# Optimization experiments

Measured on AMD Instinct MI355X. Metric: run time of the kernel, lower is better.

Reference implementation:

```python
import jax, jax.numpy as jnp
import numpy as np

EPS = 1e-10
TEMP = 1.0
N_ITERS = 21  # 20 + int(1.0 / temp)


def _sinkhorn(log_alpha, temp, n_iters):
    # log_alpha: (..., n, n). Alternating row/col log-normalization in log space.
    la = log_alpha / temp
    for _ in range(n_iters):
        la = la - jax.scipy.special.logsumexp(la, axis=-2, keepdims=True)
        la = la - jax.scipy.special.logsumexp(la, axis=-1, keepdims=True)
    return jnp.exp(la)


def setup_inputs() -> dict:
    key = jax.random.key(0)
    k1, k2, k3 = jax.random.split(key, 3)
    B, N, S = 256, 1024, 16
    x = jax.random.normal(k1, (B, N), dtype=jnp.float32)
    log_alpha = jax.random.normal(k2, (N, N), dtype=jnp.float32)  # learned param (init was gumbel noise)
    u = jax.random.uniform(k3, (S, N, N), dtype=jnp.float32)  # uniform draws for Gumbel noise
    return {"x": x, "log_alpha": log_alpha, "u": u}


def reference(x, log_alpha, u):
    # Gumbel noise from uniform draws: -log(eps - log(U + eps))
    noise = -jnp.log(EPS - jnp.log(u + EPS))  # (S, N, N)
    log_alpha_noise = log_alpha[None, :, :] + noise
    soft_perms = _sinkhorn(log_alpha_noise, TEMP, N_ITERS)  # (S, N, N)
    # x: (B, N) -> (1, B, N) @ (S, N, N) -> (S, B, N)
    return jnp.einsum('bn,snm->sbm', x, soft_perms)
```

## Files before the change

### kernel.cpp

```cpp
#include <hip/hip_runtime.h>
#include <math.h>

static constexpr int S_ = 16;
static constexpr int N_ = 1024;
static constexpr int B_ = 256;
static constexpr int ITERS = 21;
#define EPSC 1e-10f

using short8 = __attribute__((ext_vector_type(8))) short;
using f32x4  = __attribute__((ext_vector_type(4))) float;

__device__ __forceinline__ float bf2f(unsigned short h) {
    union { unsigned int u; float f; } v; v.u = ((unsigned int)h) << 16; return v.f;
}
__device__ __forceinline__ unsigned short f2bf(float f) {
    union { float f; unsigned int u; } v; v.f = f;
    unsigned int r = v.u + 0x7fffu + ((v.u >> 16) & 1u);
    return (unsigned short)(r >> 16);
}
__device__ __forceinline__ unsigned int pack2(float a, float b) {
    return (unsigned int)f2bf(a) | ((unsigned int)f2bf(b) << 16);
}

__device__ __forceinline__ float la0_of(float uv, float lav) {
    float t1 = __logf(uv + EPSC);
    float t2 = EPSC - t1;
    return lav - __logf(t2);
}

__device__ __forceinline__ void unpack16(const uint4& a, const uint4& b, float* kf) {
    kf[0]  = bf2f((unsigned short)(a.x & 0xffffu)); kf[1]  = bf2f((unsigned short)(a.x >> 16));
    kf[2]  = bf2f((unsigned short)(a.y & 0xffffu)); kf[3]  = bf2f((unsigned short)(a.y >> 16));
    kf[4]  = bf2f((unsigned short)(a.z & 0xffffu)); kf[5]  = bf2f((unsigned short)(a.z >> 16));
    kf[6]  = bf2f((unsigned short)(a.w & 0xffffu)); kf[7]  = bf2f((unsigned short)(a.w >> 16));
    kf[8]  = bf2f((unsigned short)(b.x & 0xffffu)); kf[9]  = bf2f((unsigned short)(b.x >> 16));
    kf[10] = bf2f((unsigned short)(b.y & 0xffffu)); kf[11] = bf2f((unsigned short)(b.y >> 16));
    kf[12] = bf2f((unsigned short)(b.z & 0xffffu)); kf[13] = bf2f((unsigned short)(b.z >> 16));
    kf[14] = bf2f((unsigned short)(b.w & 0xffffu)); kf[15] = bf2f((unsigned short)(b.w >> 16));
}

__global__ void __launch_bounds__(256)
build_K2(const float* __restrict__ u, const float* __restrict__ la,
         unsigned short* __restrict__ Kb, float* __restrict__ partial) {
    const int bid = blockIdx.x;
    const int s    = (bid & 7) + 8 * ((bid >> 3) & 1);
    const int slab = bid >> 4;
    const int t = threadIdx.x, wv = t >> 6, l = t & 63;
    const int i0 = slab * 8 + wv * 2;

    float cs[16];
    #pragma unroll
    for (int e = 0; e < 16; ++e) cs[e] = 0.f;

    f32x4 uu[2][4];
    float4 ll[2][4];
    #pragma unroll
    for (int rr = 0; rr < 2; ++rr) {
        const int i = i0 + rr;
        const float* up  = u  + ((size_t)s * N_ + i) * N_ + 8 * l;
        const float* lap = la + (size_t)i * N_ + 8 * l;
        uu[rr][0] = __builtin_nontemporal_load((const f32x4*)(up));
        uu[rr][1] = __builtin_nontemporal_load((const f32x4*)(up + 4));
        uu[rr][2] = __builtin_nontemporal_load((const f32x4*)(up + 512));
        uu[rr][3] = __builtin_nontemporal_load((const f32x4*)(up + 516));
        ll[rr][0] = *(const float4*)(lap);
        ll[rr][1] = *(const float4*)(lap + 4);
        ll[rr][2] = *(const float4*)(lap + 512);
        ll[rr][3] = *(const float4*)(lap + 516);
    }
    #pragma unroll
    for (int rr = 0; rr < 2; ++rr) {
        const int i = i0 + rr;
        #pragma unroll
        for (int h = 0; h < 2; ++h) {
            const float uf[8] = {uu[rr][2*h][0], uu[rr][2*h][1], uu[rr][2*h][2], uu[rr][2*h][3],
                                 uu[rr][2*h+1][0], uu[rr][2*h+1][1], uu[rr][2*h+1][2], uu[rr][2*h+1][3]};
            const float lf[8] = {ll[rr][2*h].x, ll[rr][2*h].y, ll[rr][2*h].z, ll[rr][2*h].w,
                                 ll[rr][2*h+1].x, ll[rr][2*h+1].y, ll[rr][2*h+1].z, ll[rr][2*h+1].w};
            unsigned int pk[4];
            #pragma unroll
            for (int e = 0; e < 4; ++e) {
                float k0 = __expf(lf[2*e])   / (EPSC - __logf(uf[2*e]   + EPSC));
                float k1 = __expf(lf[2*e+1]) / (EPSC - __logf(uf[2*e+1] + EPSC));
                unsigned short b0 = f2bf(k0), b1 = f2bf(k1);
                pk[e] = (unsigned int)b0 | ((unsigned int)b1 << 16);
                cs[h*8 + 2*e]     += bf2f(b0);
                cs[h*8 + 2*e + 1] += bf2f(b1);
            }
            *(uint4*)(Kb + ((size_t)s * N_ + i) * N_ + h * 512 + 8 * l) =
                make_uint4(pk[0], pk[1], pk[2], pk[3]);
        }
    }

    __shared__ float lds[4][1024];
    *(float4*)&lds[wv][8*l]           = make_float4(cs[0], cs[1], cs[2], cs[3]);
    *(float4*)&lds[wv][8*l + 4]       = make_float4(cs[4], cs[5], cs[6], cs[7]);
    *(float4*)&lds[wv][512 + 8*l]     = make_float4(cs[8], cs[9], cs[10], cs[11]);
    *(float4*)&lds[wv][512 + 8*l + 4] = make_float4(cs[12], cs[13], cs[14], cs[15]);
    __syncthreads();
    const int j = t * 4;
    float4 p0 = *(const float4*)&lds[0][j];
    float4 p1 = *(const float4*)&lds[1][j];
    float4 p2 = *(const float4*)&lds[2][j];
    float4 p3 = *(const float4*)&lds[3][j];
    float4 o;
    o.x = p0.x + p1.x + p2.x + p3.x;  o.y = p0.y + p1.y + p2.y + p3.y;
    o.z = p0.z + p1.z + p2.z + p3.z;  o.w = p0.w + p1.w + p2.w + p3.w;
    *(float4*)(partial + ((size_t)s * 128 + slab) * N_ + j) = o;
}

template<int NS>
__global__ void __launch_bounds__(256)
reduce_V(const float* __restrict__ partial, float* __restrict__ V) {
    const int s = blockIdx.x >> 2;
    const int j = (blockIdx.x & 3) * 256 + threadIdx.x;
    const float* p = partial + (size_t)s * NS * N_ + j;
    float acc = 0.f;
    #pragma unroll
    for (int q = 0; q < NS; ++q) acc += p[(size_t)q * N_];
    V[s * N_ + j] = 1.0f / acc;
}

__global__ void __launch_bounds__(256)
sink_iter(const unsigned short* __restrict__ Kb, const float* __restrict__ V,
          float* __restrict__ U, float* __restrict__ partial, int do_colsum) {
    const int bid = blockIdx.x;
    const int s    = (bid & 7) + 8 * ((bid >> 3) & 1);
    const int slab = bid >> 4;
    const int t = threadIdx.x, wv = t >> 6, l = t & 63;

    float v[16];
    const float* Vp = V + s * N_;
    *(float4*)&v[0]  = *(const float4*)(Vp + 8*l);
    *(float4*)&v[4]  = *(const float4*)(Vp + 8*l + 4);
    *(float4*)&v[8]  = *(const float4*)(Vp + 512 + 8*l);
    *(float4*)&v[12] = *(const float4*)(Vp + 512 + 8*l + 4);

    float cs[16];
    #pragma unroll
    for (int e = 0; e < 16; ++e) cs[e] = 0.f;

    const int i0 = slab * 16 + wv * 4;
    const unsigned short* rowp = Kb + ((size_t)s * N_ + i0) * N_;
    #pragma unroll
    for (int rr = 0; rr < 4; ++rr, rowp += N_) {
        uint4 ra = *(const uint4*)(rowp + 8*l);
        uint4 rb = *(const uint4*)(rowp + 512 + 8*l);
        float kf[16];
        unpack16(ra, rb, kf);
        float dot = 0.f;
        #pragma unroll
        for (int e = 0; e < 16; ++e) dot += kf[e] * v[e];
        #pragma unroll
        for (int m = 32; m >= 1; m >>= 1) dot += __shfl_xor(dot, m);
        const float ui = 1.0f / dot;
        if (l == 0) U[s * N_ + i0 + rr] = ui;
        #pragma unroll
        for (int e = 0; e < 16; ++e) cs[e] += kf[e] * ui;
    }

    if (!do_colsum) return;
    __shared__ float lds[4][1024];
    *(float4*)&lds[wv][8*l]           = make_float4(cs[0], cs[1], cs[2], cs[3]);
    *(float4*)&lds[wv][8*l + 4]       = make_float4(cs[4], cs[5], cs[6], cs[7]);
    *(float4*)&lds[wv][512 + 8*l]     = make_float4(cs[8], cs[9], cs[10], cs[11]);
    *(float4*)&lds[wv][512 + 8*l + 4] = make_float4(cs[12], cs[13], cs[14], cs[15]);
    __syncthreads();
    const int j = t * 4;
    float4 p0 = *(const float4*)&lds[0][j];
    float4 p1 = *(const float4*)&lds[1][j];
    float4 p2 = *(const float4*)&lds[2][j];
    float4 p3 = *(const float4*)&lds[3][j];
    float4 o;
    o.x = p0.x + p1.x + p2.x + p3.x;  o.y = p0.y + p1.y + p2.y + p3.y;
    o.z = p0.z + p1.z + p2.z + p3.z;  o.w = p0.w + p1.w + p2.w + p3.w;
    *(float4*)(partial + ((size_t)s * 64 + slab) * N_ + j) = o;
}

__global__ void __launch_bounds__(256)
transpose_K(const unsigned short* __restrict__ Kb, unsigned short* __restrict__ KbT) {
    const int s = blockIdx.z, k0 = blockIdx.x * 64, m0 = blockIdx.y * 64;
    __shared__ unsigned short tile[64][66];
    const int t = threadIdx.x, c4 = (t & 15) * 4, rr = t >> 4;
    const unsigned short* src = Kb + (size_t)s * N_ * N_;
    unsigned short* dst = KbT + (size_t)s * N_ * N_;
    #pragma unroll
    for (int q = 0; q < 4; ++q) {
        const int r = q * 16 + rr;
        ushort4 v = *(const ushort4*)(src + (size_t)(k0 + r) * N_ + m0 + c4);
        tile[r][c4] = v.x; tile[r][c4 + 1] = v.y; tile[r][c4 + 2] = v.z; tile[r][c4 + 3] = v.w;
    }
    __syncthreads();
    #pragma unroll
    for (int q = 0; q < 4; ++q) {
        const int rm = q * 16 + rr;
        ushort4 v;
        v.x = tile[c4][rm]; v.y = tile[c4 + 1][rm];
        v.z = tile[c4 + 2][rm]; v.w = tile[c4 + 3][rm];
        *(ushort4*)(dst + (size_t)(m0 + rm) * N_ + k0 + c4) = v;
    }
}

__global__ void __launch_bounds__(512)
mfma_out(const float* __restrict__ x, const unsigned short* __restrict__ KbT,
         const float* __restrict__ U, const float* __restrict__ V,
         float* __restrict__ out) {
    const int s  = blockIdx.z;
    const int m0 = blockIdx.x * 64;
    const int b0 = blockIdx.y * 128;
    const int t  = threadIdx.x;
    const int wid = t >> 6, l = t & 63;
    const int wr = wid & 3;
    const int wc = wid >> 2;

    __shared__ alignas(16) unsigned short lsA[128 * 64];
    __shared__ alignas(16) unsigned short lsB[64 * 64];

    f32x4 acc[2][2];
    #pragma unroll
    for (int fi = 0; fi < 2; ++fi)
        #pragma unroll
        for (int fj = 0; fj < 2; ++fj)
            acc[fi][fj] = (f32x4){0.f, 0.f, 0.f, 0.f};

    const unsigned short* Bp = KbT + ((size_t)s * N_ + m0) * N_;
    const float* Up = U + s * N_;

    float4 xa[2], xb[2];
    uint4  kv;
    float4 ua, ub;

    auto load_tile = [&](int k0) {
        #pragma unroll
        for (int i = 0; i < 2; ++i) {
            const int Lb  = i * 8192 + t * 16;
            const int row = Lb >> 7;
            const int kb  = Lb & 127;
            const float* xp = x + (size_t)(b0 + row) * N_ + k0 + (kb >> 1);
            xa[i] = *(const float4*)xp;
            xb[i] = *(const float4*)(xp + 4);
        }
        {
            const int Lb  = t * 16;
            const int row = Lb >> 7;
            const int kb  = Lb & 127;
            kv = *(const uint4*)((const char*)Bp + (size_t)row * 2048 + (k0 << 1) + kb);
            const int ke = k0 + (kb >> 1);
            ua = *(const float4*)(Up + ke);
            ub = *(const float4*)(Up + ke + 4);
        }
    };

    load_tile(0);
    for (int k0 = 0; k0 < N_; k0 += 64) {
        __syncthreads();
        #pragma unroll
        for (int i = 0; i < 2; ++i) {
            const int Lb  = i * 8192 + t * 16;
            const int row = Lb >> 7;
            const int kb  = Lb & 127;
            uint4 pk = make_uint4(pack2(xa[i].x, xa[i].y), pack2(xa[i].z, xa[i].w),
                                  pack2(xb[i].x, xb[i].y), pack2(xb[i].z, xb[i].w));
            *(uint4*)((char*)lsA + (row << 7) + (kb ^ ((row & 7) << 4))) = pk;
        }
        {
            const int Lb  = t * 16;
            const int row = Lb >> 7;
            const int kb  = Lb & 127;
            uint4 pk;
            pk.x = pack2(bf2f((unsigned short)(kv.x & 0xffffu)) * ua.x,
                         bf2f((unsigned short)(kv.x >> 16))     * ua.y);
            pk.y = pack2(bf2f((unsigned short)(kv.y & 0xffffu)) * ua.z,
                         bf2f((unsigned short)(kv.y >> 16))     * ua.w);
            pk.z = pack2(bf2f((unsigned short)(kv.z & 0xffffu)) * ub.x,
                         bf2f((unsigned short)(kv.z >> 16))     * ub.y);
            pk.w = pack2(bf2f((unsigned short)(kv.w & 0xffffu)) * ub.z,
                         bf2f((unsigned short)(kv.w >> 16))     * ub.w);
            *(uint4*)((char*)lsB + (row << 7) + (kb ^ ((row & 7) << 4))) = pk;
        }
        __syncthreads();
        if (k0 + 64 < N_) load_tile(k0 + 64);
        #pragma unroll
        for (int ks = 0; ks < 2; ++ks) {
            const int koff = ks * 64 + ((l >> 4) << 4);
            short8 afr[2], bfr[2];
            #pragma unroll
            for (int fi = 0; fi < 2; ++fi) {
                const int r = wr * 32 + fi * 16 + (l & 15);
                afr[fi] = *(const short8*)((const char*)lsA + (r << 7) + (koff ^ ((r & 7) << 4)));
            }
            #pragma unroll
            for (int fj = 0; fj < 2; ++fj) {
                const int r = wc * 32 + fj * 16 + (l & 15);
                bfr[fj] = *(const short8*)((const char*)lsB + (r << 7) + (koff ^ ((r & 7) << 4)));
            }
            #pragma unroll
            for (int fi = 0; fi < 2; ++fi)
                #pragma unroll
                for (int fj = 0; fj < 2; ++fj)
                    acc[fi][fj] = __builtin_amdgcn_mfma_f32_16x16x32_bf16(
                        afr[fi], bfr[fj], acc[fi][fj], 0, 0, 0);
        }
    }
    #pragma unroll
    for (int fj = 0; fj < 2; ++fj) {
        const int m = m0 + wc * 32 + fj * 16 + (l & 15);
        const float vm = V[s * N_ + m];
        #pragma unroll
        for (int fi = 0; fi < 2; ++fi) {
            const int b = b0 + wr * 32 + fi * 16 + ((l >> 4) << 2);
            float* op = out + ((size_t)s * B_ + b) * N_ + m;
            #pragma unroll
            for (int e = 0; e < 4; ++e)
                op[(size_t)e * N_] = acc[fi][fj][e] * vm;
        }
    }
}

__global__ void __launch_bounds__(256)
transpose_x(const float* __restrict__ x, float* __restrict__ xT) {
    __shared__ float tile[32][33];
    const int tx = threadIdx.x, ty = threadIdx.y;
    const int gx = blockIdx.x * 32, gy = blockIdx.y * 32;
    #pragma unroll
    for (int i = 0; i < 4; ++i)
        tile[ty + i * 8][tx] = x[(gy + ty + i * 8) * N_ + gx + tx];
    __syncthreads();
    #pragma unroll
    for (int i = 0; i < 4; ++i)
        xT[(size_t)(gx + ty + i * 8) * B_ + gy + tx] = tile[tx][ty + i * 8];
}

__global__ void __launch_bounds__(256)
col_pass(const float* __restrict__ u, const float* __restrict__ la,
         const float* __restrict__ r, float* __restrict__ c) {
    const int s = blockIdx.y, t = threadIdx.x;
    const int tx = t & 15, rg = t >> 4;
    const int j = blockIdx.x * 16 + tx;
    __shared__ alignas(16) float r_lds[N_];
    ((float4*)r_lds)[t] = ((const float4*)(r + s * N_))[t];
    __syncthreads();
    const float cj = c[s * N_ + j];
    const float* up = u + (size_t)s * N_ * N_;
    const int i0 = rg * 64;
    float acc = 0.f;
    #pragma unroll 4
    for (int ii = 0; ii < 64; ++ii) {
        const int i = i0 + ii;
        acc += __expf(la0_of(up[(size_t)i * N_ + j], la[i * N_ + j]) - r_lds[i] - cj);
    }
    __shared__ float sums[16][17];
    sums[rg][tx] = acc;
    __syncthreads();
    if (t < 16) {
        float tot = 0.f;
        #pragma unroll
        for (int k = 0; k < 16; ++k) tot += sums[k][t];
        c[s * N_ + blockIdx.x * 16 + t] = cj + __logf(tot);
    }
}

__global__ void __launch_bounds__(256)
row_pass(const float* __restrict__ u, const float* __restrict__ la,
         const float* __restrict__ c, float* __restrict__ r) {
    const int s = blockIdx.y, t = threadIdx.x;
    const int w = t >> 6, l = t & 63;
    const int i = blockIdx.x * 4 + w;
    __shared__ alignas(16) float c_lds[N_];
    ((float4*)c_lds)[t] = ((const float4*)(c + s * N_))[t];
    __syncthreads();
    const float ri = r[s * N_ + i];
    const float* up = u + (size_t)s * N_ * N_ + (size_t)i * N_;
    const float* lap = la + (size_t)i * N_;
    float acc = 0.f;
    #pragma unroll
    for (int k = 0; k < 16; ++k) {
        const int jj = l + (k << 6);
        acc += __expf(la0_of(up[jj], lap[jj]) - c_lds[jj] - ri);
    }
    #pragma unroll
    for (int m = 32; m >= 1; m >>= 1) acc += __shfl_xor(acc, m);
    if (l == 0) r[s * N_ + i] = ri + __logf(acc);
}

__global__ void __launch_bounds__(256)
matmul_out(const float* __restrict__ u, const float* __restrict__ la,
           const float* __restrict__ xT, const float* __restrict__ r,
           const float* __restrict__ c, float* __restrict__ out) {
    const int s = blockIdx.z, m0 = blockIdx.x * 64, b0 = blockIdx.y * 128;
    const int t = threadIdx.x, tx = t & 7, ty = t >> 3;
    __shared__ alignas(16) float Bs[16][64];
    float acc[4][8] = {};
    const float* up = u + (size_t)s * N_ * N_;
    const float* rp = r + s * N_;
    for (int k0 = 0; k0 < N_; k0 += 16) {
        __syncthreads();
        {
            const int kk = t >> 4, f4 = t & 15;
            const int k = k0 + kk;
            const float rk = rp[k];
            const float4 uv = *(const float4*)(up + (size_t)k * N_ + m0 + f4 * 4);
            const float4 lv = *(const float4*)(la + (size_t)k * N_ + m0 + f4 * 4);
            float4 p;
            p.x = __expf(la0_of(uv.x, lv.x) - rk);
            p.y = __expf(la0_of(uv.y, lv.y) - rk);
            p.z = __expf(la0_of(uv.z, lv.z) - rk);
            p.w = __expf(la0_of(uv.w, lv.w) - rk);
            *(float4*)(&Bs[kk][f4 * 4]) = p;
        }
        __syncthreads();
        #pragma unroll
        for (int kk = 0; kk < 16; ++kk) {
            const float4 a4 = *(const float4*)(xT + (size_t)(k0 + kk) * B_ + b0 + ty * 4);
            const float4 bA = *(const float4*)(&Bs[kk][tx * 8]);
            const float4 bB = *(const float4*)(&Bs[kk][tx * 8 + 4]);
            const float av[4] = {a4.x, a4.y, a4.z, a4.w};
            const float bv[8] = {bA.x, bA.y, bA.z, bA.w, bB.x, bB.y, bB.z, bB.w};
            #pragma unroll
            for (int rr = 0; rr < 4; ++rr)
                #pragma unroll
                for (int cc = 0; cc < 8; ++cc)
                    acc[rr][cc] += av[rr] * bv[cc];
        }
    }
    float cm[8];
    #pragma unroll
    for (int cc = 0; cc < 8; ++cc) cm[cc] = __expf(-c[s * N_ + m0 + tx * 8 + cc]);
    #pragma unroll
    for (int rr = 0; rr < 4; ++rr) {
        float4 o0, o1;
        o0.x = acc[rr][0] * cm[0]; o0.y = acc[rr][1] * cm[1];
        o0.z = acc[rr][2] * cm[2]; o0.w = acc[rr][3] * cm[3];
        o1.x = acc[rr][4] * cm[4]; o1.y = acc[rr][5] * cm[5];
        o1.z = acc[rr][6] * cm[6]; o1.w = acc[rr][7] * cm[7];
        float* op = out + ((size_t)s * B_ + b0 + ty * 4 + rr) * N_ + m0 + tx * 8;
        *(float4*)op       = o0;
        *(float4*)(op + 4) = o1;
    }
}

extern "C" void kernel_launch(void* const* d_in, const int* in_sizes, int n_in,
                              void* d_out, int out_size, void* d_ws, size_t ws_size,
                              hipStream_t stream) {
    (void)in_sizes; (void)n_in; (void)out_size;
    const float* x  = (const float*)d_in[0];
    const float* la = (const float*)d_in[1];
    const float* u  = (const float*)d_in[2];
    float* out = (float*)d_out;

    const size_t KN = (size_t)S_ * N_ * N_;
    const size_t need = KN * 2 * 2
                      + (size_t)2 * S_ * N_ * 4;

    if (ws_size >= need) {
        unsigned short* Kb  = (unsigned short*)d_ws;
        unsigned short* KbT = Kb + KN;
        float* partial = (float*)KbT;
        float* U = (float*)(KbT + KN);
        float* V = U + S_ * N_;

        build_K2<<<2048, 256, 0, stream>>>(u, la, Kb, partial);

        for (int it = 0; it < ITERS; ++it) {
            if (it == 0) reduce_V<128><<<64, 256, 0, stream>>>(partial, V);
            else         reduce_V<64><<<64, 256, 0, stream>>>(partial, V);
            sink_iter<<<1024, 256, 0, stream>>>(Kb, V, U, partial,
                                                it == ITERS - 1 ? 0 : 1);
        }

        transpose_K<<<dim3(16, 16, 16), 256, 0, stream>>>(Kb, KbT);

        mfma_out<<<dim3(N_ / 64, B_ / 128, S_), 512, 0, stream>>>(x, KbT, U, V, out);
    } else {
        float* r  = (float*)d_ws;
        float* c  = r + S_ * N_;
        float* xT = c + S_ * N_;
        (void)hipMemsetAsync(d_ws, 0, 2 * S_ * N_ * sizeof(float), stream);
        transpose_x<<<dim3(N_ / 32, B_ / 32), dim3(32, 8), 0, stream>>>(x, xT);
        for (int it = 0; it < ITERS; ++it) {
            col_pass<<<dim3(N_ / 16, S_), 256, 0, stream>>>(u, la, r, c);
            row_pass<<<dim3(N_ / 4, S_),  256, 0, stream>>>(u, la, c, r);
        }
        matmul_out<<<dim3(N_ / 64, B_ / 128, S_), 256, 0, stream>>>(u, la, xT, r, c, out);
    }
}
```

Before: 302.9 us.

## Fold V column-sum reduction into producer kernels via last-block atomic ticket

Removes the separate reduce_V launches after build_K2 and after each Sinkhorn iteration. Each block now writes its partial column sums and takes an agent-scope atomic ticket on a per-sample counter. The last-arriving block for that sample sums all partials and writes the reciprocal V. This saves about 21 small kernel launches and their gaps, at the cost of a counter memset, atomics, and a serial tail reduction in one block per sample. It also depends on the acquire/release semantics making other blocks' partial writes visible across XCD caches.

```diff
diff --git a/kernel.cpp b/kernel.cpp
--- a/kernel.cpp
+++ b/kernel.cpp
@@ -39,9 +39,37 @@
     kf[14] = bf2f((unsigned short)(b.w & 0xffffu)); kf[15] = bf2f((unsigned short)(b.w >> 16));
 }
 
+__device__ __forceinline__ bool ticket_last(unsigned int* cnt, unsigned int expected) {
+    __shared__ int lastf;
+    __syncthreads();
+    if (threadIdx.x == 0) {
+        unsigned int old = __hip_atomic_fetch_add(cnt, 1u, __ATOMIC_ACQ_REL,
+                                                  __HIP_MEMORY_SCOPE_AGENT);
+        lastf = (old == expected - 1u);
+    }
+    __syncthreads();
+    return lastf != 0;
+}
+
+template<int NS>
+__device__ __forceinline__ void finish_V(const float* __restrict__ pbase,
+                                         float* __restrict__ Vp) {
+    const int t = threadIdx.x;
+    const float* p = pbase + t * 4;
+    float4 acc = make_float4(0.f, 0.f, 0.f, 0.f);
+    #pragma unroll
+    for (int q = 0; q < NS; ++q) {
+        float4 v = *(const float4*)(p + (size_t)q * N_);
+        acc.x += v.x; acc.y += v.y; acc.z += v.z; acc.w += v.w;
+    }
+    float4 o = make_float4(1.f / acc.x, 1.f / acc.y, 1.f / acc.z, 1.f / acc.w);
+    *(float4*)(Vp + t * 4) = o;
+}
+
 __global__ void __launch_bounds__(256)
 build_K2(const float* __restrict__ u, const float* __restrict__ la,
-         unsigned short* __restrict__ Kb, float* __restrict__ partial) {
+         unsigned short* __restrict__ Kb, float* __restrict__ partial,
+         float* __restrict__ V, unsigned int* __restrict__ cnt) {
     const int bid = blockIdx.x;
     const int s    = (bid & 7) + 8 * ((bid >> 3) & 1);
     const int slab = bid >> 4;
@@ -106,24 +134,18 @@
     float4 o;
     o.x = p0.x + p1.x + p2.x + p3.x;  o.y = p0.y + p1.y + p2.y + p3.y;
     o.z = p0.z + p1.z + p2.z + p3.z;  o.w = p0.w + p1.w + p2.w + p3.w;
-    *(float4*)(partial + ((size_t)s * 128 + slab) * N_ + j) = o;
-}
-
-template<int NS>
-__global__ void __launch_bounds__(256)
-reduce_V(const float* __restrict__ partial, float* __restrict__ V) {
-    const int s = blockIdx.x >> 2;
-    const int j = (blockIdx.x & 3) * 256 + threadIdx.x;
-    const float* p = partial + (size_t)s * NS * N_ + j;
-    float acc = 0.f;
-    #pragma unroll
-    for (int q = 0; q < NS; ++q) acc += p[(size_t)q * N_];
-    V[s * N_ + j] = 1.0f / acc;
+    float* pbase = partial + (size_t)s * 128 * N_;
+    *(float4*)(pbase + (size_t)slab * N_ + j) = o;
+
+    if (ticket_last(cnt + s, 128))
+        finish_V<128>(pbase, V + s * N_);
 }
 
 __global__ void __launch_bounds__(256)
 sink_iter(const unsigned short* __restrict__ Kb, const float* __restrict__ V,
-          float* __restrict__ U, float* __restrict__ partial, int do_colsum) {
+          float* __restrict__ U, float* __restrict__ partial,
+          float* __restrict__ Vnext, unsigned int* __restrict__ cnt,
+          int do_colsum) {
     const int bid = blockIdx.x;
     const int s    = (bid & 7) + 8 * ((bid >> 3) & 1);
     const int slab = bid >> 4;
@@ -174,7 +196,11 @@
     float4 o;
     o.x = p0.x + p1.x + p2.x + p3.x;  o.y = p0.y + p1.y + p2.y + p3.y;
     o.z = p0.z + p1.z + p2.z + p3.z;  o.w = p0.w + p1.w + p2.w + p3.w;
-    *(float4*)(partial + ((size_t)s * 64 + slab) * N_ + j) = o;
+    float* pbase = partial + (size_t)s * 64 * N_;
+    *(float4*)(pbase + (size_t)slab * N_ + j) = o;
+
+    if (ticket_last(cnt + s, 64))
+        finish_V<64>(pbase, Vnext + s * N_);
 }
 
 __global__ void __launch_bounds__(256)
@@ -449,8 +475,10 @@
     float* out = (float*)d_out;
 
     const size_t KN = (size_t)S_ * N_ * N_;
+    const size_t CNT_WORDS = (size_t)(1 + ITERS) * S_;
     const size_t need = KN * 2 * 2
-                      + (size_t)2 * S_ * N_ * 4;
+                      + (size_t)2 * S_ * N_ * 4
+                      + CNT_WORDS * 4;
 
     if (ws_size >= need) {
         unsigned short* Kb  = (unsigned short*)d_ws;
@@ -458,13 +486,15 @@
         float* partial = (float*)KbT;
         float* U = (float*)(KbT + KN);
         float* V = U + S_ * N_;
-
-        build_K2<<<2048, 256, 0, stream>>>(u, la, Kb, partial);
+        unsigned int* cnt = (unsigned int*)(V + S_ * N_);
+
+        (void)hipMemsetAsync(cnt, 0, CNT_WORDS * 4, stream);
+
+        build_K2<<<2048, 256, 0, stream>>>(u, la, Kb, partial, V, cnt);
 
         for (int it = 0; it < ITERS; ++it) {
-            if (it == 0) reduce_V<128><<<64, 256, 0, stream>>>(partial, V);
-            else         reduce_V<64><<<64, 256, 0, stream>>>(partial, V);
-            sink_iter<<<1024, 256, 0, stream>>>(Kb, V, U, partial,
+            sink_iter<<<1024, 256, 0, stream>>>(Kb, V, U, partial, V,
+                                                cnt + (size_t)(1 + it) * S_,
                                                 it == ITERS - 1 ? 0 : 1);
         }
 
```

After: 992.2 us. 3.28x slower.
